# Optimization experiments

Hardware: AMD Instinct MI355X
Metric: run time of the kernel (lower is better)

The kernel has to match this reference:

```python
import jax, jax.numpy as jnp
import numpy as np

B, S, D, H = 2, 2048, 1024, 16
HD = D // H
NEG_INF = jnp.finfo(jnp.float32).min


def setup_inputs() -> dict:
    key = jax.random.key(0)
    ks = jax.random.split(key, 6)
    s = 1.0 / np.sqrt(D)
    return {
        'x': jax.random.normal(ks[0], (B, S, D), dtype=jnp.float32),
        'Wq': jax.random.normal(ks[1], (D, D), dtype=jnp.float32) * s,
        'Wk': jax.random.normal(ks[2], (D, D), dtype=jnp.float32) * s,
        'Wv': jax.random.normal(ks[3], (D, D), dtype=jnp.float32) * s,
        'Wo': jax.random.normal(ks[4], (D, D), dtype=jnp.float32) * s,
        'bo': jnp.zeros((D,), dtype=jnp.float32),
    }


def reference(x, Wq, Wk, Wv, Wo, bo):
    b, s, _ = x.shape
    scale = HD ** -0.5
    # Q/K/V projections: einsum('bnd,di->bni') == x @ W
    def proj(W):
        return jnp.einsum('bnd,di->bni', x, W).reshape(b, s, H, HD).transpose(0, 2, 1, 3)
    Q, K, V = proj(Wq), proj(Wk), proj(Wv)  # [b,h,s,hd]
    scores = jnp.einsum('bhnd,bhmd->bhnm', Q, K) * scale  # [b,h,s,s]
    causal = jnp.tril(jnp.ones((s, s), dtype=bool))
    scores = jnp.where(causal[None, None], scores, NEG_INF)
    attn = jax.nn.softmax(scores, axis=-1)
    ctx = jnp.einsum('bhnm,bhmd->bhnd', attn, V)
    ctx = ctx.transpose(0, 2, 1, 3).reshape(b, s, D)
    # nn.Linear: ctx @ Wo.T + bo
    return jnp.einsum('bnd,od->bno', ctx, Wo) + bo
```

## Files before the change

### kernel.cpp

```cpp
#include <hip/hip_runtime.h>

#define B_  2
#define S_  2048
#define D_  1024
#define H_  16
#define HD_ 64
#define M_  (B_*S_)

typedef __attribute__((ext_vector_type(8))) short s16x8;
typedef __attribute__((ext_vector_type(4))) float f32x4;
typedef __attribute__((ext_vector_type(16))) float f32x16;

__device__ __forceinline__ unsigned short f2bf(float f) {
  unsigned int u = __builtin_bit_cast(unsigned int, f);
  u += 0x7fffu + ((u >> 16) & 1u);
  return (unsigned short)(u >> 16);
}
__device__ __forceinline__ float bf2f(unsigned short h) {
  unsigned int u = ((unsigned int)h) << 16;
  return __builtin_bit_cast(float, u);
}

__device__ __forceinline__ void gload_lds16(const unsigned short* g, unsigned short* l) {
  __builtin_amdgcn_global_load_lds((const __attribute__((address_space(1))) void*)g,
                                   (__attribute__((address_space(3))) void*)l, 16, 0, 0);
}

__global__ void cvt_kernel(const float* __restrict__ in, unsigned short* __restrict__ out, int n4) {
  int i = blockIdx.x * blockDim.x + threadIdx.x;
  if (i >= n4) return;
  float4 v = reinterpret_cast<const float4*>(in)[i];
  ushort4 o;
  o.x = f2bf(v.x); o.y = f2bf(v.y); o.z = f2bf(v.z); o.w = f2bf(v.w);
  reinterpret_cast<ushort4*>(out)[i] = o;
}

__global__ void transpose_cvt3(const float* __restrict__ W0, const float* __restrict__ W1,
                               const float* __restrict__ W2, unsigned short* __restrict__ dstBase) {
  __shared__ float tile[32][33];
  const float* in = blockIdx.z == 0 ? W0 : (blockIdx.z == 1 ? W1 : W2);
  unsigned short* out = dstBase + (size_t)blockIdx.z * 1024 * 1024;
  const int bx = blockIdx.x, by = blockIdx.y, tx = threadIdx.x;
  const int x = bx * 32 + tx;
  for (int j = threadIdx.y; j < 32; j += 8)
    tile[j][tx] = in[(by * 32 + j) * 1024 + x];
  __syncthreads();
  const int xo = by * 32 + tx;
  for (int j = threadIdx.y; j < 32; j += 8)
    out[(bx * 32 + j) * 1024 + xo] = f2bf(tile[tx][j]);
}

#define BM 128
#define BN 128
#define BK 64

__global__ __launch_bounds__(256, 4) void gemm_bt(
    const unsigned short* __restrict__ A,
    const unsigned short* __restrict__ Bt,
    void* __restrict__ out0, void* __restrict__ out1, void* __restrict__ out2,
    const float* __restrict__ bias,
    const int mode, const float qscale)
{
  __shared__ unsigned short As[BM * BK];
  __shared__ unsigned short Bs[BN * BK];

  const int t    = threadIdx.x;
  const int lane = t & 63;
  const int wid  = t >> 6;
  const int l15  = lane & 15;
  const int g    = lane >> 4;
  const int wm   = wid >> 1;
  const int wn   = wid & 1;

  const int n0 = blockIdx.x * BN;
  const int m0 = blockIdx.y * BM;

  const int lrow = lane >> 3;
  const int lcol = ((lane & 7) ^ lrow) * 8;
  const int rsw  = l15 & 7;

  f32x4 acc[4][4];
#pragma unroll
  for (int i = 0; i < 4; ++i)
#pragma unroll
    for (int j = 0; j < 4; ++j)
      acc[i][j] = (f32x4){0.f, 0.f, 0.f, 0.f};

  for (int kt = 0; kt < 1024 / BK; ++kt) {
    const int k0 = kt * BK;
#pragma unroll
    for (int p = 0; p < 4; ++p) {
      const int c = p * 4 + wid;
      const int row = c * 8 + lrow;
      gload_lds16(&A[(size_t)(m0 + row) * 1024 + k0 + lcol], &As[c * 512]);
      gload_lds16(&Bt[(size_t)(n0 + row) * 1024 + k0 + lcol], &Bs[c * 512]);
    }
    __syncthreads();

#pragma unroll
    for (int kk = 0; kk < 2; ++kk) {
      s16x8 af[4], bf[4];
#pragma unroll
      for (int mi = 0; mi < 4; ++mi)
        af[mi] = *reinterpret_cast<const s16x8*>(
            &As[(wm * 64 + mi * 16 + l15) * BK + (((4 * kk + g) ^ rsw) * 8)]);
#pragma unroll
      for (int ni = 0; ni < 4; ++ni)
        bf[ni] = *reinterpret_cast<const s16x8*>(
            &Bs[(wn * 64 + ni * 16 + l15) * BK + (((4 * kk + g) ^ rsw) * 8)]);
#pragma unroll
      for (int mi = 0; mi < 4; ++mi)
#pragma unroll
        for (int ni = 0; ni < 4; ++ni)
          acc[mi][ni] = __builtin_amdgcn_mfma_f32_16x16x32_bf16(af[mi], bf[ni], acc[mi][ni], 0, 0, 0);
    }
    __syncthreads();
  }

  if (mode == 0) {
    const int sel = n0 >> 10;
    const int nl0 = n0 & 1023;
    if (sel < 2) {
      unsigned short* outb = (unsigned short*)(sel == 0 ? out0 : out1);
      const float sc = (sel == 0) ? qscale : 1.0f;
#pragma unroll
      for (int mi = 0; mi < 4; ++mi) {
#pragma unroll
        for (int ni = 0; ni < 4; ++ni) {
          const int n = nl0 + wn * 64 + ni * 16 + l15;
          const int h = n >> 6, hd = n & 63;
#pragma unroll
          for (int r = 0; r < 4; ++r) {
            const int m = m0 + wm * 64 + mi * 16 + 4 * g + r;
            const int b = m >> 11, s = m & 2047;
            outb[(((b * H_ + h) * S_) + s) * HD_ + hd] = f2bf(acc[mi][ni][r] * sc);
          }
        }
      }
    } else {
      unsigned short* outb = (unsigned short*)out2;
#pragma unroll
      for (int mi = 0; mi < 4; ++mi) {
#pragma unroll
        for (int ni = 0; ni < 4; ++ni) {
          const int n = nl0 + wn * 64 + ni * 16 + l15;
          const int h = n >> 6, hd = n & 63;
          const int m = m0 + wm * 64 + mi * 16 + 4 * g;
          const int b = m >> 11, s = m & 2047;
          ushort4 o;
          o.x = f2bf(acc[mi][ni][0]);
          o.y = f2bf(acc[mi][ni][1]);
          o.z = f2bf(acc[mi][ni][2]);
          o.w = f2bf(acc[mi][ni][3]);
          *reinterpret_cast<ushort4*>(&outb[(((b * H_ + h) * HD_) + hd) * S_ + s]) = o;
        }
      }
    }
  } else {
    float* outf = (float*)out0;
#pragma unroll
    for (int mi = 0; mi < 4; ++mi) {
#pragma unroll
      for (int ni = 0; ni < 4; ++ni) {
        const int n = n0 + wn * 64 + ni * 16 + l15;
        const float bv = bias[n];
#pragma unroll
        for (int r = 0; r < 4; ++r) {
          const int m = m0 + wm * 64 + mi * 16 + 4 * g + r;
          outf[m * 1024 + n] = acc[mi][ni][r] + bv;
        }
      }
    }
  }
}

__global__ __launch_bounds__(256, 4) void attn_kernel(
    const unsigned short* __restrict__ Q,
    const unsigned short* __restrict__ K,
    const unsigned short* __restrict__ VT,
    unsigned short* __restrict__ Ctx,
    unsigned short* __restrict__ pctx,
    float* __restrict__ pml)
{
  __shared__ unsigned short Vl[2][64 * 64];
  __shared__ unsigned short Pl[4][2][32][40];

  static const unsigned char QBv[24] = {15,15,7,14,14,13,13,6,12,12,11,11,5,10,10,9,9,4,8,8,3,2,1,0};
  static const signed char   HFv[24] = {0,1,-1,0,1,0,1,-1,0,1,0,1,-1,0,1,0,1,-1,0,1,-1,-1,-1,-1};

  const int t    = threadIdx.x;
  const int lane = t & 63;
  const int w    = t >> 6;
  const int q    = lane & 31;
  const int hi   = lane >> 5;

  const int bh = blockIdx.x;
  const int qb = QBv[blockIdx.y];
  const int hf = HFv[blockIdx.y];
  const long base  = (long)bh * S_ * HD_;
  const long vbase = (long)bh * HD_ * S_;
  const int q0w = qb * 128 + w * 32;

  int ktBeg, ktEnd;
  if (hf < 0) { ktBeg = 0; ktEnd = 2 * qb + 2; }
  else        { ktBeg = hf * (qb + 1); ktEnd = ktBeg + qb + 1; }

  const int srow = lane >> 3;
  const int scol = ((lane & 7) ^ srow) * 8;
  const int swz  = (q & 7) * 8;

  s16x8 qf[4];
#pragma unroll
  for (int s = 0; s < 4; ++s)
    qf[s] = *reinterpret_cast<const s16x8*>(&Q[base + (long)(q0w + q) * HD_ + 16 * s + 8 * hi]);

  f32x16 ctx0, ctx1;
#pragma unroll
  for (int r = 0; r < 16; ++r) { ctx0[r] = 0.f; ctx1[r] = 0.f; }
  float m_run = -1e30f, l_run = 0.f;

#pragma unroll
  for (int p = 0; p < 2; ++p) {
    const int c = 2 * w + p;
    gload_lds16(&VT[vbase + (long)(c * 8 + srow) * S_ + ktBeg * 64 + scol], &Vl[0][c * 512]);
  }
  __syncthreads();

  for (int kt = ktBeg; kt < ktEnd; ++kt) {
    const int cur  = (kt - ktBeg) & 1;
    const int kv64 = kt * 64;

    if (kt + 1 < ktEnd) {
      const int nk = (kt + 1) * 64;
#pragma unroll
      for (int p = 0; p < 2; ++p) {
        const int c = 2 * w + p;
        gload_lds16(&VT[vbase + (long)(c * 8 + srow) * S_ + nk + scol], &Vl[cur ^ 1][c * 512]);
      }
    }

    if (kv64 <= q0w + 31) {
      const unsigned short* Kt = &K[base + (long)kv64 * HD_];
      s16x8 kb0[4], kb1[4];
#pragma unroll
      for (int s = 0; s < 4; ++s) {
        kb0[s] = *reinterpret_cast<const s16x8*>(&Kt[(q) * HD_ + 16 * s + 8 * hi]);
        kb1[s] = *reinterpret_cast<const s16x8*>(&Kt[(32 + q) * HD_ + 16 * s + 8 * hi]);
      }

      f32x16 sa0, sa1;
#pragma unroll
      for (int r = 0; r < 16; ++r) { sa0[r] = 0.f; sa1[r] = 0.f; }
      __builtin_amdgcn_s_setprio(1);
#pragma unroll
      for (int s = 0; s < 4; ++s)
        sa0 = __builtin_amdgcn_mfma_f32_32x32x16_bf16(kb0[s], qf[s], sa0, 0, 0, 0);
#pragma unroll
      for (int s = 0; s < 4; ++s)
        sa1 = __builtin_amdgcn_mfma_f32_32x32x16_bf16(kb1[s], qf[s], sa1, 0, 0, 0);
      __builtin_amdgcn_s_setprio(0);

      if (kv64 + 64 > q0w) {
#pragma unroll
        for (int r = 0; r < 16; ++r) {
          const int kl = (r & 3) + 8 * (r >> 2) + 4 * hi;
          if (kv64 + kl > q0w + q)      sa0[r] = -1e30f;
          if (kv64 + 32 + kl > q0w + q) sa1[r] = -1e30f;
        }
      }

      float mx;
      {
        float a0 = fmaxf(fmaxf(sa0[0], sa0[1]), fmaxf(sa0[2], sa0[3]));
        float a1 = fmaxf(fmaxf(sa0[4], sa0[5]), fmaxf(sa0[6], sa0[7]));
        float a2 = fmaxf(fmaxf(sa0[8], sa0[9]), fmaxf(sa0[10], sa0[11]));
        float a3 = fmaxf(fmaxf(sa0[12], sa0[13]), fmaxf(sa0[14], sa0[15]));
        float b0 = fmaxf(fmaxf(sa1[0], sa1[1]), fmaxf(sa1[2], sa1[3]));
        float b1 = fmaxf(fmaxf(sa1[4], sa1[5]), fmaxf(sa1[6], sa1[7]));
        float b2 = fmaxf(fmaxf(sa1[8], sa1[9]), fmaxf(sa1[10], sa1[11]));
        float b3 = fmaxf(fmaxf(sa1[12], sa1[13]), fmaxf(sa1[14], sa1[15]));
        mx = fmaxf(fmaxf(fmaxf(a0, a1), fmaxf(a2, a3)), fmaxf(fmaxf(b0, b1), fmaxf(b2, b3)));
        mx = fmaxf(mx, __shfl_xor(mx, 32));
      }
      if (mx > m_run + 8.f) {
        const float alpha = __builtin_amdgcn_exp2f(m_run - mx);
        m_run = mx;
        l_run *= alpha;
#pragma unroll
        for (int r = 0; r < 16; ++r) { ctx0[r] *= alpha; ctx1[r] *= alpha; }
      }

      float p0[16], p1[16];
#pragma unroll
      for (int r = 0; r < 16; ++r) {
        p0[r] = __builtin_amdgcn_exp2f(sa0[r] - m_run);
        p1[r] = __builtin_amdgcn_exp2f(sa1[r] - m_run);
      }
      float ps;
      {
        float s0 = ((p0[0] + p0[1]) + (p0[2] + p0[3])) + ((p0[4] + p0[5]) + (p0[6] + p0[7]));
        float s1 = ((p0[8] + p0[9]) + (p0[10] + p0[11])) + ((p0[12] + p0[13]) + (p0[14] + p0[15]));
        float s2 = ((p1[0] + p1[1]) + (p1[2] + p1[3])) + ((p1[4] + p1[5]) + (p1[6] + p1[7]));
        float s3 = ((p1[8] + p1[9]) + (p1[10] + p1[11])) + ((p1[12] + p1[13]) + (p1[14] + p1[15]));
        ps = (s0 + s1) + (s2 + s3);
        ps += __shfl_xor(ps, 32);
      }
      l_run += ps;

#pragma unroll
      for (int c = 0; c < 4; ++c) {
        unsigned int pk01, pk23;
        asm("v_cvt_pk_bf16_f32 %0, %1, %2" : "=v"(pk01) : "v"(p0[4 * c + 0]), "v"(p0[4 * c + 1]));
        asm("v_cvt_pk_bf16_f32 %0, %1, %2" : "=v"(pk23) : "v"(p0[4 * c + 2]), "v"(p0[4 * c + 3]));
        uint2 pr; pr.x = pk01; pr.y = pk23;
        *reinterpret_cast<uint2*>(&Pl[w][0][q][8 * c + 4 * hi]) = pr;
      }
#pragma unroll
      for (int c = 0; c < 4; ++c) {
        unsigned int pk01, pk23;
        asm("v_cvt_pk_bf16_f32 %0, %1, %2" : "=v"(pk01) : "v"(p1[4 * c + 0]), "v"(p1[4 * c + 1]));
        asm("v_cvt_pk_bf16_f32 %0, %1, %2" : "=v"(pk23) : "v"(p1[4 * c + 2]), "v"(p1[4 * c + 3]));
        uint2 pr; pr.x = pk01; pr.y = pk23;
        *reinterpret_cast<uint2*>(&Pl[w][1][q][8 * c + 4 * hi]) = pr;
      }

      __builtin_amdgcn_s_setprio(1);
#pragma unroll
      for (int kc = 0; kc < 4; ++kc) {
        const s16x8 pf = *reinterpret_cast<const s16x8*>(&Pl[w][kc >> 1][q][16 * (kc & 1) + 8 * hi]);
        const s16x8 v0 = *reinterpret_cast<const s16x8*>(&Vl[cur][(q) * 64 + ((16 * kc + 8 * hi) ^ swz)]);
        ctx0 = __builtin_amdgcn_mfma_f32_32x32x16_bf16(v0, pf, ctx0, 0, 0, 0);
        const s16x8 v1 = *reinterpret_cast<const s16x8*>(&Vl[cur][(32 + q) * 64 + ((16 * kc + 8 * hi) ^ swz)]);
        ctx1 = __builtin_amdgcn_mfma_f32_32x32x16_bf16(v1, pf, ctx1, 0, 0, 0);
      }
      __builtin_amdgcn_s_setprio(0);
    }

    __syncthreads();
  }

  if (hf < 0) {
    const int b = bh >> 4, h = bh & 15;
    const float inv = 1.f / l_run;
    unsigned short* orow = &Ctx[((long)b * S_ + q0w + q) * D_ + h * 64];
#pragma unroll
    for (int c = 0; c < 4; ++c) {
      ushort4 o0, o1;
      o0.x = f2bf(ctx0[4 * c] * inv);     o0.y = f2bf(ctx0[4 * c + 1] * inv);
      o0.z = f2bf(ctx0[4 * c + 2] * inv); o0.w = f2bf(ctx0[4 * c + 3] * inv);
      o1.x = f2bf(ctx1[4 * c] * inv);     o1.y = f2bf(ctx1[4 * c + 1] * inv);
      o1.z = f2bf(ctx1[4 * c + 2] * inv); o1.w = f2bf(ctx1[4 * c + 3] * inv);
      *reinterpret_cast<ushort4*>(&orow[8 * c + 4 * hi])      = o0;
      *reinterpret_cast<ushort4*>(&orow[32 + 8 * c + 4 * hi]) = o1;
    }
  } else {
    const int sidx = ((bh << 3) + (qb - 8)) * 2 + hf;
    const int rloc = w * 32 + q;
    unsigned short* prow = &pctx[((long)sidx * 128 + rloc) * 64];
#pragma unroll
    for (int c = 0; c < 4; ++c) {
      ushort4 o0, o1;
      o0.x = f2bf(ctx0[4 * c]);     o0.y = f2bf(ctx0[4 * c + 1]);
      o0.z = f2bf(ctx0[4 * c + 2]); o0.w = f2bf(ctx0[4 * c + 3]);
      o1.x = f2bf(ctx1[4 * c]);     o1.y = f2bf(ctx1[4 * c + 1]);
      o1.z = f2bf(ctx1[4 * c + 2]); o1.w = f2bf(ctx1[4 * c + 3]);
      *reinterpret_cast<ushort4*>(&prow[8 * c + 4 * hi])      = o0;
      *reinterpret_cast<ushort4*>(&prow[32 + 8 * c + 4 * hi]) = o1;
    }
    if (hi == 0) {
      pml[((long)sidx * 128 + rloc) * 2]     = m_run;
      pml[((long)sidx * 128 + rloc) * 2 + 1] = l_run;
    }
  }
}

__global__ __launch_bounds__(256) void merge_kernel(
    const unsigned short* __restrict__ pctx,
    const float* __restrict__ pml,
    unsigned short* __restrict__ Ctx)
{
  const int unit = blockIdx.x;
  const int bh = unit >> 3;
  const int qb = (unit & 7) + 8;
  const long s0 = (long)unit * 2, s1 = s0 + 1;

  const int t   = threadIdx.x;
  const int row = t >> 1;
  const int hh  = t & 1;

  const long r0 = s0 * 128 + row;
  const long r1 = s1 * 128 + row;
  const float m0 = pml[r0 * 2], l0 = pml[r0 * 2 + 1];
  const float m1 = pml[r1 * 2], l1 = pml[r1 * 2 + 1];
  const float M  = fmaxf(m0, m1);
  const float a0 = __builtin_amdgcn_exp2f(m0 - M);
  const float a1 = __builtin_amdgcn_exp2f(m1 - M);
  const float inv = 1.f / (l0 * a0 + l1 * a1);

  const unsigned short* c0p = &pctx[r0 * 64 + hh * 32];
  const unsigned short* c1p = &pctx[r1 * 64 + hh * 32];
  const int b = bh >> 4, h = bh & 15;
  unsigned short* op = &Ctx[((long)b * S_ + qb * 128 + row) * D_ + h * 64 + hh * 32];

#pragma unroll
  for (int j = 0; j < 32; j += 8) {
    const s16x8 v0 = *reinterpret_cast<const s16x8*>(&c0p[j]);
    const s16x8 v1 = *reinterpret_cast<const s16x8*>(&c1p[j]);
    s16x8 o;
#pragma unroll
    for (int e = 0; e < 8; ++e) {
      const float f = (bf2f((unsigned short)v0[e]) * a0 + bf2f((unsigned short)v1[e]) * a1) * inv;
      o[e] = (short)f2bf(f);
    }
    *reinterpret_cast<s16x8*>(&op[j]) = o;
  }
}

extern "C" void kernel_launch(void* const* d_in, const int* in_sizes, int n_in,
                              void* d_out, int out_size, void* d_ws, size_t ws_size,
                              hipStream_t stream) {
  const float* x  = (const float*)d_in[0];
  const float* Wq = (const float*)d_in[1];
  const float* Wk = (const float*)d_in[2];
  const float* Wv = (const float*)d_in[3];
  const float* Wo = (const float*)d_in[4];
  const float* bo = (const float*)d_in[5];
  float* out = (float*)d_out;

  char* ws = (char*)d_ws;
  const size_t MB = 1024 * 1024;
  unsigned short* xb  = (unsigned short*)(ws + 0 * MB);
  unsigned short* WT  = (unsigned short*)(ws + 8 * MB);
  unsigned short* Wob = (unsigned short*)(ws + 14 * MB);
  unsigned short* Qb  = (unsigned short*)(ws + 16 * MB);
  unsigned short* Kb  = (unsigned short*)(ws + 24 * MB);
  unsigned short* VTb = (unsigned short*)(ws + 32 * MB);
  unsigned short* Cx  = (unsigned short*)(ws + 40 * MB);
  unsigned short* pctx = (unsigned short*)(ws + 0 * MB);
  float*          pml  = (float*)(ws + 8 * MB);

  cvt_kernel<<<(M_ * D_ / 4 + 255) / 256, 256, 0, stream>>>(x, xb, M_ * D_ / 4);
  cvt_kernel<<<(D_ * D_ / 4 + 255) / 256, 256, 0, stream>>>(Wo, Wob, D_ * D_ / 4);
  transpose_cvt3<<<dim3(32, 32, 3), dim3(32, 8), 0, stream>>>(Wq, Wk, Wv, WT);

  gemm_bt<<<dim3(3 * D_ / BN, M_ / BM), 256, 0, stream>>>(
      xb, WT, (void*)Qb, (void*)Kb, (void*)VTb, nullptr, 0, 0.18033688011112042f);

  attn_kernel<<<dim3(B_ * H_, 24), 256, 0, stream>>>(Qb, Kb, VTb, Cx, pctx, pml);
  merge_kernel<<<256, 256, 0, stream>>>(pctx, pml, Cx);

  gemm_bt<<<dim3(D_ / BN, M_ / BM), 256, 0, stream>>>(
      Cx, Wob, (void*)out, nullptr, nullptr, bo, 1, 1.0f);
}
```

Baseline: 117.9 us.

## Load V fragments directly from global per wave, drop shared V tile and block barriers

Replaces the block-shared, double-buffered V^T tile in LDS (filled with global_load_lds and guarded by __syncthreads every iteration) with per-wave direct global loads of V fragments into registers alongside the K loads. Waves now break out of the key loop independently once past the causal diagonal instead of idling through barriers. This removes the per-iteration block barrier and the LDS footprint for V, which may raise occupancy. In exchange each wave reads V from global/L2 separately, with strided rows of length S, so redundant global traffic rises and the prefetch overlap is lost.

```diff
diff --git a/kernel.cpp b/kernel.cpp
--- a/kernel.cpp
+++ b/kernel.cpp
@@ -182,7 +182,6 @@
     unsigned short* __restrict__ pctx,
     float* __restrict__ pml)
 {
-  __shared__ unsigned short Vl[2][64 * 64];
   __shared__ unsigned short Pl[4][2][32][40];
 
   static const unsigned char QBv[24] = {15,15,7,14,14,13,13,6,12,12,11,11,5,10,10,9,9,4,8,8,3,2,1,0};
@@ -205,10 +204,6 @@
   if (hf < 0) { ktBeg = 0; ktEnd = 2 * qb + 2; }
   else        { ktBeg = hf * (qb + 1); ktEnd = ktBeg + qb + 1; }
 
-  const int srow = lane >> 3;
-  const int scol = ((lane & 7) ^ srow) * 8;
-  const int swz  = (q & 7) * 8;
-
   s16x8 qf[4];
 #pragma unroll
   for (int s = 0; s < 4; ++s)
@@ -219,124 +214,105 @@
   for (int r = 0; r < 16; ++r) { ctx0[r] = 0.f; ctx1[r] = 0.f; }
   float m_run = -1e30f, l_run = 0.f;
 
-#pragma unroll
-  for (int p = 0; p < 2; ++p) {
-    const int c = 2 * w + p;
-    gload_lds16(&VT[vbase + (long)(c * 8 + srow) * S_ + ktBeg * 64 + scol], &Vl[0][c * 512]);
-  }
-  __syncthreads();
-
   for (int kt = ktBeg; kt < ktEnd; ++kt) {
-    const int cur  = (kt - ktBeg) & 1;
     const int kv64 = kt * 64;
-
-    if (kt + 1 < ktEnd) {
-      const int nk = (kt + 1) * 64;
-#pragma unroll
-      for (int p = 0; p < 2; ++p) {
-        const int c = 2 * w + p;
-        gload_lds16(&VT[vbase + (long)(c * 8 + srow) * S_ + nk + scol], &Vl[cur ^ 1][c * 512]);
+    if (kv64 > q0w + 31) break;
+
+    const unsigned short* Kt = &K[base + (long)kv64 * HD_];
+    const unsigned short* Vp = &VT[vbase + kv64];
+    s16x8 kb0[4], kb1[4], vf0[4], vf1[4];
+#pragma unroll
+    for (int s = 0; s < 4; ++s) {
+      kb0[s] = *reinterpret_cast<const s16x8*>(&Kt[(q) * HD_ + 16 * s + 8 * hi]);
+      kb1[s] = *reinterpret_cast<const s16x8*>(&Kt[(32 + q) * HD_ + 16 * s + 8 * hi]);
+      vf0[s] = *reinterpret_cast<const s16x8*>(&Vp[(long)(q) * S_ + 16 * s + 8 * hi]);
+      vf1[s] = *reinterpret_cast<const s16x8*>(&Vp[(long)(32 + q) * S_ + 16 * s + 8 * hi]);
+    }
+
+    f32x16 sa0, sa1;
+#pragma unroll
+    for (int r = 0; r < 16; ++r) { sa0[r] = 0.f; sa1[r] = 0.f; }
+    __builtin_amdgcn_s_setprio(1);
+#pragma unroll
+    for (int s = 0; s < 4; ++s)
+      sa0 = __builtin_amdgcn_mfma_f32_32x32x16_bf16(kb0[s], qf[s], sa0, 0, 0, 0);
+#pragma unroll
+    for (int s = 0; s < 4; ++s)
+      sa1 = __builtin_amdgcn_mfma_f32_32x32x16_bf16(kb1[s], qf[s], sa1, 0, 0, 0);
+    __builtin_amdgcn_s_setprio(0);
+
+    if (kv64 + 64 > q0w) {
+#pragma unroll
+      for (int r = 0; r < 16; ++r) {
+        const int kl = (r & 3) + 8 * (r >> 2) + 4 * hi;
+        if (kv64 + kl > q0w + q)      sa0[r] = -1e30f;
+        if (kv64 + 32 + kl > q0w + q) sa1[r] = -1e30f;
       }
     }
 
-    if (kv64 <= q0w + 31) {
-      const unsigned short* Kt = &K[base + (long)kv64 * HD_];
-      s16x8 kb0[4], kb1[4];
-#pragma unroll
-      for (int s = 0; s < 4; ++s) {
-        kb0[s] = *reinterpret_cast<const s16x8*>(&Kt[(q) * HD_ + 16 * s + 8 * hi]);
-        kb1[s] = *reinterpret_cast<const s16x8*>(&Kt[(32 + q) * HD_ + 16 * s + 8 * hi]);
-      }
-
-      f32x16 sa0, sa1;
-#pragma unroll
-      for (int r = 0; r < 16; ++r) { sa0[r] = 0.f; sa1[r] = 0.f; }
-      __builtin_amdgcn_s_setprio(1);
-#pragma unroll
-      for (int s = 0; s < 4; ++s)
-        sa0 = __builtin_amdgcn_mfma_f32_32x32x16_bf16(kb0[s], qf[s], sa0, 0, 0, 0);
-#pragma unroll
-      for (int s = 0; s < 4; ++s)
-        sa1 = __builtin_amdgcn_mfma_f32_32x32x16_bf16(kb1[s], qf[s], sa1, 0, 0, 0);
-      __builtin_amdgcn_s_setprio(0);
-
-      if (kv64 + 64 > q0w) {
-#pragma unroll
-        for (int r = 0; r < 16; ++r) {
-          const int kl = (r & 3) + 8 * (r >> 2) + 4 * hi;
-          if (kv64 + kl > q0w + q)      sa0[r] = -1e30f;
-          if (kv64 + 32 + kl > q0w + q) sa1[r] = -1e30f;
-        }
-      }
-
-      float mx;
-      {
-        float a0 = fmaxf(fmaxf(sa0[0], sa0[1]), fmaxf(sa0[2], sa0[3]));
-        float a1 = fmaxf(fmaxf(sa0[4], sa0[5]), fmaxf(sa0[6], sa0[7]));
-        float a2 = fmaxf(fmaxf(sa0[8], sa0[9]), fmaxf(sa0[10], sa0[11]));
-        float a3 = fmaxf(fmaxf(sa0[12], sa0[13]), fmaxf(sa0[14], sa0[15]));
-        float b0 = fmaxf(fmaxf(sa1[0], sa1[1]), fmaxf(sa1[2], sa1[3]));
-        float b1 = fmaxf(fmaxf(sa1[4], sa1[5]), fmaxf(sa1[6], sa1[7]));
-        float b2 = fmaxf(fmaxf(sa1[8], sa1[9]), fmaxf(sa1[10], sa1[11]));
-        float b3 = fmaxf(fmaxf(sa1[12], sa1[13]), fmaxf(sa1[14], sa1[15]));
-        mx = fmaxf(fmaxf(fmaxf(a0, a1), fmaxf(a2, a3)), fmaxf(fmaxf(b0, b1), fmaxf(b2, b3)));
-        mx = fmaxf(mx, __shfl_xor(mx, 32));
-      }
-      if (mx > m_run + 8.f) {
-        const float alpha = __builtin_amdgcn_exp2f(m_run - mx);
-        m_run = mx;
-        l_run *= alpha;
-#pragma unroll
-        for (int r = 0; r < 16; ++r) { ctx0[r] *= alpha; ctx1[r] *= alpha; }
-      }
-
-      float p0[16], p1[16];
-#pragma unroll
-      for (int r = 0; r < 16; ++r) {
-        p0[r] = __builtin_amdgcn_exp2f(sa0[r] - m_run);
-        p1[r] = __builtin_amdgcn_exp2f(sa1[r] - m_run);
-      }
-      float ps;
-      {
-        float s0 = ((p0[0] + p0[1]) + (p0[2] + p0[3])) + ((p0[4] + p0[5]) + (p0[6] + p0[7]));
-        float s1 = ((p0[8] + p0[9]) + (p0[10] + p0[11])) + ((p0[12] + p0[13]) + (p0[14] + p0[15]));
-        float s2 = ((p1[0] + p1[1]) + (p1[2] + p1[3])) + ((p1[4] + p1[5]) + (p1[6] + p1[7]));
-        float s3 = ((p1[8] + p1[9]) + (p1[10] + p1[11])) + ((p1[12] + p1[13]) + (p1[14] + p1[15]));
-        ps = (s0 + s1) + (s2 + s3);
-        ps += __shfl_xor(ps, 32);
-      }
-      l_run += ps;
-
-#pragma unroll
-      for (int c = 0; c < 4; ++c) {
-        unsigned int pk01, pk23;
-        asm("v_cvt_pk_bf16_f32 %0, %1, %2" : "=v"(pk01) : "v"(p0[4 * c + 0]), "v"(p0[4 * c + 1]));
-        asm("v_cvt_pk_bf16_f32 %0, %1, %2" : "=v"(pk23) : "v"(p0[4 * c + 2]), "v"(p0[4 * c + 3]));
-        uint2 pr; pr.x = pk01; pr.y = pk23;
-        *reinterpret_cast<uint2*>(&Pl[w][0][q][8 * c + 4 * hi]) = pr;
-      }
-#pragma unroll
-      for (int c = 0; c < 4; ++c) {
-        unsigned int pk01, pk23;
-        asm("v_cvt_pk_bf16_f32 %0, %1, %2" : "=v"(pk01) : "v"(p1[4 * c + 0]), "v"(p1[4 * c + 1]));
-        asm("v_cvt_pk_bf16_f32 %0, %1, %2" : "=v"(pk23) : "v"(p1[4 * c + 2]), "v"(p1[4 * c + 3]));
-        uint2 pr; pr.x = pk01; pr.y = pk23;
-        *reinterpret_cast<uint2*>(&Pl[w][1][q][8 * c + 4 * hi]) = pr;
-      }
-
-      __builtin_amdgcn_s_setprio(1);
-#pragma unroll
-      for (int kc = 0; kc < 4; ++kc) {
-        const s16x8 pf = *reinterpret_cast<const s16x8*>(&Pl[w][kc >> 1][q][16 * (kc & 1) + 8 * hi]);
-        const s16x8 v0 = *reinterpret_cast<const s16x8*>(&Vl[cur][(q) * 64 + ((16 * kc + 8 * hi) ^ swz)]);
-        ctx0 = __builtin_amdgcn_mfma_f32_32x32x16_bf16(v0, pf, ctx0, 0, 0, 0);
-        const s16x8 v1 = *reinterpret_cast<const s16x8*>(&Vl[cur][(32 + q) * 64 + ((16 * kc + 8 * hi) ^ swz)]);
-        ctx1 = __builtin_amdgcn_mfma_f32_32x32x16_bf16(v1, pf, ctx1, 0, 0, 0);
-      }
-      __builtin_amdgcn_s_setprio(0);
-    }
-
-    __syncthreads();
+    float mx;
+    {
+      float a0 = fmaxf(fmaxf(sa0[0], sa0[1]), fmaxf(sa0[2], sa0[3]));
+      float a1 = fmaxf(fmaxf(sa0[4], sa0[5]), fmaxf(sa0[6], sa0[7]));
+      float a2 = fmaxf(fmaxf(sa0[8], sa0[9]), fmaxf(sa0[10], sa0[11]));
+      float a3 = fmaxf(fmaxf(sa0[12], sa0[13]), fmaxf(sa0[14], sa0[15]));
+      float b0 = fmaxf(fmaxf(sa1[0], sa1[1]), fmaxf(sa1[2], sa1[3]));
+      float b1 = fmaxf(fmaxf(sa1[4], sa1[5]), fmaxf(sa1[6], sa1[7]));
+      float b2 = fmaxf(fmaxf(sa1[8], sa1[9]), fmaxf(sa1[10], sa1[11]));
+      float b3 = fmaxf(fmaxf(sa1[12], sa1[13]), fmaxf(sa1[14], sa1[15]));
+      mx = fmaxf(fmaxf(fmaxf(a0, a1), fmaxf(a2, a3)), fmaxf(fmaxf(b0, b1), fmaxf(b2, b3)));
+      mx = fmaxf(mx, __shfl_xor(mx, 32));
+    }
+    if (mx > m_run + 8.f) {
+      const float alpha = __builtin_amdgcn_exp2f(m_run - mx);
+      m_run = mx;
+      l_run *= alpha;
+#pragma unroll
+      for (int r = 0; r < 16; ++r) { ctx0[r] *= alpha; ctx1[r] *= alpha; }
+    }
+
+    float p0[16], p1[16];
+#pragma unroll
+    for (int r = 0; r < 16; ++r) {
+      p0[r] = __builtin_amdgcn_exp2f(sa0[r] - m_run);
+      p1[r] = __builtin_amdgcn_exp2f(sa1[r] - m_run);
+    }
+    float ps;
+    {
+      float s0 = ((p0[0] + p0[1]) + (p0[2] + p0[3])) + ((p0[4] + p0[5]) + (p0[6] + p0[7]));
+      float s1 = ((p0[8] + p0[9]) + (p0[10] + p0[11])) + ((p0[12] + p0[13]) + (p0[14] + p0[15]));
+      float s2 = ((p1[0] + p1[1]) + (p1[2] + p1[3])) + ((p1[4] + p1[5]) + (p1[6] + p1[7]));
+      float s3 = ((p1[8] + p1[9]) + (p1[10] + p1[11])) + ((p1[12] + p1[13]) + (p1[14] + p1[15]));
+      ps = (s0 + s1) + (s2 + s3);
+      ps += __shfl_xor(ps, 32);
+    }
+    l_run += ps;
+
+#pragma unroll
+    for (int c = 0; c < 4; ++c) {
+      unsigned int pk01, pk23;
+      asm("v_cvt_pk_bf16_f32 %0, %1, %2" : "=v"(pk01) : "v"(p0[4 * c + 0]), "v"(p0[4 * c + 1]));
+      asm("v_cvt_pk_bf16_f32 %0, %1, %2" : "=v"(pk23) : "v"(p0[4 * c + 2]), "v"(p0[4 * c + 3]));
+      uint2 pr; pr.x = pk01; pr.y = pk23;
+      *reinterpret_cast<uint2*>(&Pl[w][0][q][8 * c + 4 * hi]) = pr;
+    }
+#pragma unroll
+    for (int c = 0; c < 4; ++c) {
+      unsigned int pk01, pk23;
+      asm("v_cvt_pk_bf16_f32 %0, %1, %2" : "=v"(pk01) : "v"(p1[4 * c + 0]), "v"(p1[4 * c + 1]));
+      asm("v_cvt_pk_bf16_f32 %0, %1, %2" : "=v"(pk23) : "v"(p1[4 * c + 2]), "v"(p1[4 * c + 3]));
+      uint2 pr; pr.x = pk01; pr.y = pk23;
+      *reinterpret_cast<uint2*>(&Pl[w][1][q][8 * c + 4 * hi]) = pr;
+    }
+
+    __builtin_amdgcn_s_setprio(1);
+#pragma unroll
+    for (int kc = 0; kc < 4; ++kc) {
+      const s16x8 pf = *reinterpret_cast<const s16x8*>(&Pl[w][kc >> 1][q][16 * (kc & 1) + 8 * hi]);
+      ctx0 = __builtin_amdgcn_mfma_f32_32x32x16_bf16(vf0[kc], pf, ctx0, 0, 0, 0);
+      ctx1 = __builtin_amdgcn_mfma_f32_32x32x16_bf16(vf1[kc], pf, ctx1, 0, 0, 0);
+    }
+    __builtin_amdgcn_s_setprio(0);
   }
 
   if (hf < 0) {
```

New measurement: 181.2 us. 1.54x slower.
